# Kernel tuning notes

Measured on AMD Instinct MI355X. Metric: run time of the kernel, lower is better.

Reference implementation:

```python
import jax, jax.numpy as jnp
import numpy as np

T, B, S = 128, 128, 128
H, E, V, L = 1024, 512, 32000, 2


def setup_inputs() -> dict:
    key = jax.random.key(0)
    ks = jax.random.split(key, 16)
    s = 0.02
    inp = {
        "inputs": jax.random.randint(ks[0], (T, B), 0, V),
        "h0": jax.random.normal(ks[1], (L, B, H), jnp.float32) * 0.1,
        "c0": jax.random.normal(ks[2], (L, B, H), jnp.float32) * 0.1,
        "contexts": jax.random.normal(ks[3], (B, S, H), jnp.float32),
        "emb": jax.random.normal(ks[4], (V, E), jnp.float32) * s,
        "W_ih0": jax.random.normal(ks[5], (4 * H, E), jnp.float32) * s,
        "W_hh0": jax.random.normal(ks[6], (4 * H, H), jnp.float32) * s,
        "b_ih0": jnp.zeros((4 * H,), jnp.float32),
        "b_hh0": jnp.zeros((4 * H,), jnp.float32),
        "W_ih1": jax.random.normal(ks[7], (4 * H, H), jnp.float32) * s,
        "W_hh1": jax.random.normal(ks[8], (4 * H, H), jnp.float32) * s,
        "b_ih1": jnp.zeros((4 * H,), jnp.float32),
        "b_hh1": jnp.zeros((4 * H,), jnp.float32),
        "att_in_W": jax.random.normal(ks[9], (H, H), jnp.float32) * s,
        "att_in_b": jnp.zeros((H,), jnp.float32),
        "att_out_W": jax.random.normal(ks[10], (H, 2 * H), jnp.float32) * s,
        "att_out_b": jnp.zeros((H,), jnp.float32),
    }
    return inp


def _lstm_cell(x, h, c, Wih, Whh, bih, bhh):
    # torch.nn.LSTMCell: gates in (i, f, g, o) order
    gates = x @ Wih.T + bih + h @ Whh.T + bhh  # [B, 4H]
    i, f, g, o = jnp.split(gates, 4, axis=-1)
    c2 = jax.nn.sigmoid(f) * c + jax.nn.sigmoid(i) * jnp.tanh(g)
    h2 = jax.nn.sigmoid(o) * jnp.tanh(c2)
    return h2, c2


def reference(inputs, h0, c0, contexts, emb,
              W_ih0, W_hh0, b_ih0, b_hh0,
              W_ih1, W_hh1, b_ih1, b_hh1,
              att_in_W, att_in_b, att_out_W, att_out_b):
    layer_params = [(W_ih0, W_hh0, b_ih0, b_hh0), (W_ih1, W_hh1, b_ih1, b_hh1)]
    embs = emb[inputs]  # [T, B, E]

    def step(carry, x_t):
        h, c = carry  # each [L, B, H]
        x = x_t
        hs, cs = [], []
        for l, (Wih, Whh, bih, bhh) in enumerate(layer_params):
            h_l, c_l = _lstm_cell(x, h[l], c[l], Wih, Whh, bih, bhh)
            x = h_l  # dropout=0.0 / eval mode -> identity
            hs.append(h_l)
            cs.append(c_l)
        # global (Luong general) attention
        gamma = x @ att_in_W.T + att_in_b                     # [B, H]
        scores = jnp.einsum('bsh,bh->bs', contexts, gamma)    # [B, S]
        w = jax.nn.softmax(scores, axis=-1)
        c_t = jnp.einsum('bs,bsh->bh', w, contexts)           # [B, H]
        out = jnp.tanh(jnp.concatenate([c_t, x], axis=-1) @ att_out_W.T + att_out_b)
        return (jnp.stack(hs), jnp.stack(cs)), (out, w)

    (hT, cT), (outputs, attns) = jax.lax.scan(step, (h0, c0), embs)
    return outputs, hT, cT
```

## Files before the change

### kernel.cpp

```cpp
#include <hip/hip_runtime.h>

#define TT 128
#define BB 128
#define SS 128
#define HH 1024
#define EE 512
#define BH (BB*HH)

typedef unsigned short u16;
typedef unsigned long long u64;
typedef __attribute__((ext_vector_type(8))) short s8v;
typedef __attribute__((ext_vector_type(4))) float f32x4;

__device__ __forceinline__ float b2f(u16 u) {
    union { unsigned int i; float f; } v; v.i = ((unsigned int)u) << 16; return v.f;
}
__device__ __forceinline__ u16 f2b(float f) {
    union { float f; unsigned int i; } v; v.f = f;
    unsigned int x = v.i;
    x = x + 0x7fffu + ((x >> 16) & 1u);
    return (u16)(x >> 16);
}
__device__ __forceinline__ float sigm(float x) {
    float t = __expf(-fabsf(x));
    float p = 1.0f / (1.0f + t);
    return x >= 0.0f ? p : 1.0f - p;
}
__device__ __forceinline__ float tanh_(float x) {
    float t = __expf(-2.0f * fabsf(x));
    float r = (1.0f - t) / (1.0f + t);
    return x >= 0.0f ? r : -r;
}

#define MFMA(a, b, c) __builtin_amdgcn_mfma_f32_16x16x32_bf16((a), (b), (c), 0, 0, 0)

__global__ __launch_bounds__(256)
void cvt_k(const float* __restrict__ s, u16* __restrict__ d, int n)
{
    const int i = (blockIdx.x * 256 + threadIdx.x) * 4;
    if (i < n) {
        const float4 v = *(const float4*)(s + i);
        ushort4 o;
        o.x = f2b(v.x); o.y = f2b(v.y); o.z = f2b(v.z); o.w = f2b(v.w);
        *(ushort4*)(d + i) = o;
    }
}

__global__ __launch_bounds__(128)
void gather_k(const int* __restrict__ toks, const float* __restrict__ emb,
              u16* __restrict__ X)
{
    const int row = blockIdx.x;
    const int tok = toks[row];
    const int c = threadIdx.x * 4;
    const float4 v = *(const float4*)(emb + (size_t)tok * EE + c);
    ushort4 o;
    o.x = f2b(v.x); o.y = f2b(v.y); o.z = f2b(v.z); o.w = f2b(v.w);
    *(ushort4*)(X + (size_t)row * EE + c) = o;
}

__global__ __launch_bounds__(256)
void init_k(const float* __restrict__ h0in,
            u16* __restrict__ h0ring, u16* __restrict__ h1init,
            int* __restrict__ barcnt)
{
    const int i = blockIdx.x * 256 + threadIdx.x;
    const u16 hb = f2b(h0in[i]);
    if (i < BH) h0ring[i] = hb;
    else        h1init[i - BH] = hb;
    if (i < 256) barcnt[i] = 0;
}

__global__ __launch_bounds__(512, 1)
void scan_k(const float* __restrict__ Wih0, const float* __restrict__ Whh0,
            const float* __restrict__ Wih1, const float* __restrict__ Whh1,
            const float* __restrict__ bih0, const float* __restrict__ bhh0,
            const float* __restrict__ bih1, const float* __restrict__ bhh1,
            const float* __restrict__ c0in,
            const u16* __restrict__ Xb,
            u16* __restrict__ h0ring,
            const u16* __restrict__ h1init,
            u16* __restrict__ H1all,
            float* __restrict__ outT,
            int* __restrict__ barcnt)
{
    extern __shared__ u16 lds[];
    u16* W0x = lds;
    u16* W0h = W0x + 16*4*16*8;
    u16* W1x = W0h + 32*4*16*8;
    u16* W1h = W1x + 32*4*16*8;
    float* gst0 = (float*)(W1h + 32*4*16*8);
    float* gst1 = gst0 + 8*16*20;

    const int tid  = threadIdx.x;
    const int bk   = blockIdx.x;
    const int j0   = (((bk & 7) << 5) | (bk >> 3)) * 4;
    const int lane = tid & 63;
    const int w    = tid >> 6;
    const int l15  = lane & 15, quad = lane >> 4;

    auto loadW = [&](const float* src, int K, u16* dst) {
        const int ntup = (K / 32) * 4 * 16;
        for (int idx = tid; idx < ntup; idx += 512) {
            const int n = idx & 15, q = (idx >> 4) & 3, kc = idx >> 6;
            const int col = ((n >> 2) * HH) + j0 + (n & 3);
            const float* sp = src + (size_t)col * K + kc * 32 + q * 8;
            const float4 v0 = *(const float4*)(sp);
            const float4 v1 = *(const float4*)(sp + 4);
            u16* dp = dst + (size_t)idx * 8;
            dp[0] = f2b(v0.x); dp[1] = f2b(v0.y); dp[2] = f2b(v0.z); dp[3] = f2b(v0.w);
            dp[4] = f2b(v1.x); dp[5] = f2b(v1.y); dp[6] = f2b(v1.z); dp[7] = f2b(v1.w);
        }
    };
    loadW(Wih0, EE, W0x);
    loadW(Whh0, HH, W0h);
    loadW(Wih1, HH, W1x);
    loadW(Whh1, HH, W1h);

    const int pr = tid & 127;
    f32x4 cst = (f32x4)0.0f;
    f32x4 bs0 = (f32x4)0.0f, bs1 = (f32x4)0.0f, bs2 = (f32x4)0.0f, bs3 = (f32x4)0.0f;
    if (tid < 256) {
        const int layer = tid >> 7;
        const float* bi = layer ? bih1 : bih0;
        const float* bh = layer ? bhh1 : bhh0;
        cst = *(const f32x4*)(c0in + (size_t)layer * BH + (size_t)pr * HH + j0);
        bs0 = *(const f32x4*)(bi + 0 * HH + j0) + *(const f32x4*)(bh + 0 * HH + j0);
        bs1 = *(const f32x4*)(bi + 1 * HH + j0) + *(const f32x4*)(bh + 1 * HH + j0);
        bs2 = *(const f32x4*)(bi + 2 * HH + j0) + *(const f32x4*)(bh + 2 * HH + j0);
        bs3 = *(const f32x4*)(bi + 3 * HH + j0) + *(const f32x4*)(bh + 3 * HH + j0);
    }

    __syncthreads();

    const int arow = w * 16 + l15;

    #define BIDX(kc) (((size_t)((kc) * 4 + quad) * 16 + l15) * 8)

    auto pointwise = [&](const float* gbase, u16* dst, float* oH, float* oC,
                         bool doOut) {
        const float* gr = gbase + (pr >> 4) * 320 + (pr & 15) * 20;
        const f32x4 vi = *(const f32x4*)(gr + 0);
        const f32x4 vf = *(const f32x4*)(gr + 4);
        const f32x4 vg = *(const f32x4*)(gr + 8);
        const f32x4 vo = *(const f32x4*)(gr + 12);
        f32x4 hv;
        #pragma unroll
        for (int jj = 0; jj < 4; ++jj) {
            const float gi = vi[jj] + bs0[jj];
            const float gf = vf[jj] + bs1[jj];
            const float gg = vg[jj] + bs2[jj];
            const float go = vo[jj] + bs3[jj];
            const float c = sigm(gf) * cst[jj] + sigm(gi) * tanh_(gg);
            cst[jj] = c;
            hv[jj] = sigm(go) * tanh_(c);
        }
        const u64 pk = (u64)f2b(hv[0]) | ((u64)f2b(hv[1]) << 16)
                     | ((u64)f2b(hv[2]) << 32) | ((u64)f2b(hv[3]) << 48);
        __hip_atomic_store((u64*)(dst + (size_t)pr * HH + j0), pk,
                           __ATOMIC_RELAXED, __HIP_MEMORY_SCOPE_AGENT);
        if (doOut) {
            *(f32x4*)(oH + (size_t)pr * HH + j0) = hv;
            *(f32x4*)(oC + (size_t)pr * HH + j0) = cst;
        }
    };

    for (int p = 0; p <= TT; ++p) {
        f32x4 acc0 = (f32x4)0.0f, acc1 = (f32x4)0.0f;

        if (p < TT) {
            const u16* ap = Xb + ((size_t)p * BB + arow) * EE + quad * 8;
            #pragma unroll 8
            for (int kc = 0; kc < 16; ++kc) {
                s8v a = *(const s8v*)(ap + kc * 32);
                s8v b = *(const s8v*)(W0x + BIDX(kc));
                acc0 = MFMA(a, b, acc0);
            }
        }

        if (p > 0) {
            if (tid < 8) {
                const int target = 32 * p;
                while (__hip_atomic_load(barcnt + tid * 32, __ATOMIC_RELAXED,
                                         __HIP_MEMORY_SCOPE_AGENT) < target) {
                    __builtin_amdgcn_s_sleep(1);
                }
            }
            __syncthreads();
            asm volatile("" ::: "memory");
        }

        const u16* h0p = h0ring + (size_t)p * BH;
        const u16* a0p = h0p + (size_t)arow * HH + quad * 8;
        if (p == 0) {
            #pragma unroll 8
            for (int kc = 0; kc < 32; ++kc) {
                s8v a = *(const s8v*)(a0p + kc * 32);
                acc0 = MFMA(a, *(const s8v*)(W0h + BIDX(kc)), acc0);
            }
        } else {
            const u16* h1p = (p == 1) ? h1init : (H1all + (size_t)(p - 2) * BH);
            const u16* a1p = h1p + (size_t)arow * HH + quad * 8;
            if (p < TT) {
                #pragma unroll 8
                for (int kc = 0; kc < 32; ++kc) {
                    s8v a0 = *(const s8v*)(a0p + kc * 32);
                    s8v a1 = *(const s8v*)(a1p + kc * 32);
                    acc0 = MFMA(a0, *(const s8v*)(W0h + BIDX(kc)), acc0);
                    acc1 = MFMA(a0, *(const s8v*)(W1x + BIDX(kc)), acc1);
                    acc1 = MFMA(a1, *(const s8v*)(W1h + BIDX(kc)), acc1);
                }
            } else {
                #pragma unroll 8
                for (int kc = 0; kc < 32; ++kc) {
                    s8v a0 = *(const s8v*)(a0p + kc * 32);
                    s8v a1 = *(const s8v*)(a1p + kc * 32);
                    acc1 = MFMA(a0, *(const s8v*)(W1x + BIDX(kc)), acc1);
                    acc1 = MFMA(a1, *(const s8v*)(W1h + BIDX(kc)), acc1);
                }
            }
        }

        if (p < TT) {
            #pragma unroll
            for (int r = 0; r < 4; ++r)
                gst0[w * 320 + (quad * 4 + r) * 20 + l15] = acc0[r];
        }
        if (p > 0) {
            #pragma unroll
            for (int r = 0; r < 4; ++r)
                gst1[w * 320 + (quad * 4 + r) * 20 + l15] = acc1[r];
        }
        __syncthreads();
        if (p < TT && tid < 128)
            pointwise(gst0, h0ring + (size_t)(p + 1) * BH,
                      outT + (size_t)0 * BH, outT + (size_t)2 * BH, p == TT - 1);
        if (p > 0 && tid >= 128 && tid < 256)
            pointwise(gst1, H1all + (size_t)(p - 1) * BH,
                      outT + (size_t)1 * BH, outT + (size_t)3 * BH, p == TT);
        __syncthreads();

        if (p < TT && tid == 0) {
            __hip_atomic_fetch_add(barcnt + (bk & 7) * 32, 1, __ATOMIC_RELAXED,
                                   __HIP_MEMORY_SCOPE_AGENT);
        }
    }
    #undef BIDX
}

__global__ __launch_bounds__(256)
void gemm_bt_k(const u16* __restrict__ A1, int K1,
               const u16* __restrict__ A2, int K2,
               const u16* __restrict__ W, int ldw,
               const float* __restrict__ bias,
               u16* __restrict__ Cb, float* __restrict__ Cf,
               int N, int act)
{
    const int lane = threadIdx.x & 63;
    const int wave = threadIdx.x >> 6;
    const int l15 = lane & 15, quad = lane >> 4;
    const int n0 = blockIdx.x * 64;
    const int mrow = blockIdx.y * 64 + wave * 16;
    const int arow = mrow + l15;

    f32x4 acc[4];
    #pragma unroll
    for (int nt = 0; nt < 4; ++nt) acc[nt] = (f32x4)0.0f;

    const u16* wr0 = W + (size_t)(n0 + 0 * 16 + l15) * ldw + quad * 8;
    const u16* wr1 = W + (size_t)(n0 + 1 * 16 + l15) * ldw + quad * 8;
    const u16* wr2 = W + (size_t)(n0 + 2 * 16 + l15) * ldw + quad * 8;
    const u16* wr3 = W + (size_t)(n0 + 3 * 16 + l15) * ldw + quad * 8;

    {
        const u16* ap = A1 + (size_t)arow * K1 + quad * 8;
        #pragma unroll 4
        for (int kk = 0; kk < K1; kk += 32) {
            s8v a = *(const s8v*)(ap + kk);
            acc[0] = MFMA(a, *(const s8v*)(wr0 + kk), acc[0]);
            acc[1] = MFMA(a, *(const s8v*)(wr1 + kk), acc[1]);
            acc[2] = MFMA(a, *(const s8v*)(wr2 + kk), acc[2]);
            acc[3] = MFMA(a, *(const s8v*)(wr3 + kk), acc[3]);
        }
    }
    if (A2 != nullptr) {
        const u16* ap = A2 + (size_t)arow * K2 + quad * 8;
        #pragma unroll 4
        for (int kk = 0; kk < K2; kk += 32) {
            s8v a = *(const s8v*)(ap + kk);
            acc[0] = MFMA(a, *(const s8v*)(wr0 + K1 + kk), acc[0]);
            acc[1] = MFMA(a, *(const s8v*)(wr1 + K1 + kk), acc[1]);
            acc[2] = MFMA(a, *(const s8v*)(wr2 + K1 + kk), acc[2]);
            acc[3] = MFMA(a, *(const s8v*)(wr3 + K1 + kk), acc[3]);
        }
    }
    #pragma unroll
    for (int nt = 0; nt < 4; ++nt) {
        const int col = n0 + nt * 16 + l15;
        const float bv = bias[col];
        #pragma unroll
        for (int r = 0; r < 4; ++r) {
            const int row = mrow + quad * 4 + r;
            float v = acc[nt][r] + bv;
            if (act) v = tanh_(v);
            if (Cf) Cf[(size_t)row * N + col] = v;
            else    Cb[(size_t)row * N + col] = f2b(v);
        }
    }
}

__global__ __launch_bounds__(256)
void attn_k(const u16* __restrict__ gamma, const float* __restrict__ ctx,
            u16* __restrict__ ctall)
{
    const int b = blockIdx.x;
    const int t0 = blockIdx.y * 16;
    const int tid = threadIdx.x;
    const int lane = tid & 63, wave = tid >> 6;
    const int l15 = lane & 15, quad = lane >> 4;

    __shared__ float sw[16 * SS];

    {
        f32x4 acc0 = (f32x4)0.0f, acc1 = (f32x4)0.0f;
        const u16*   ap  = gamma + ((size_t)(t0 + l15) * BB + b) * HH + quad * 8;
        const float* bp0 = ctx + ((size_t)b * SS + (wave * 32 + l15)) * HH + quad * 8;
        const float* bp1 = ctx + ((size_t)b * SS + (wave * 32 + 16 + l15)) * HH + quad * 8;
        for (int kk = 0; kk < HH; kk += 32) {
            s8v a = *(const s8v*)(ap + kk);
            float4 u0 = *(const float4*)(bp0 + kk);
            float4 u1 = *(const float4*)(bp0 + kk + 4);
            s8v bv;
            bv[0] = (short)f2b(u0.x); bv[1] = (short)f2b(u0.y);
            bv[2] = (short)f2b(u0.z); bv[3] = (short)f2b(u0.w);
            bv[4] = (short)f2b(u1.x); bv[5] = (short)f2b(u1.y);
            bv[6] = (short)f2b(u1.z); bv[7] = (short)f2b(u1.w);
            acc0 = MFMA(a, bv, acc0);
            float4 w0 = *(const float4*)(bp1 + kk);
            float4 w1 = *(const float4*)(bp1 + kk + 4);
            s8v cv;
            cv[0] = (short)f2b(w0.x); cv[1] = (short)f2b(w0.y);
            cv[2] = (short)f2b(w0.z); cv[3] = (short)f2b(w0.w);
            cv[4] = (short)f2b(w1.x); cv[5] = (short)f2b(w1.y);
            cv[6] = (short)f2b(w1.z); cv[7] = (short)f2b(w1.w);
            acc1 = MFMA(a, cv, acc1);
        }
        #pragma unroll
        for (int r = 0; r < 4; ++r) {
            const int trow = quad * 4 + r;
            sw[trow * SS + wave * 32 + l15] = acc0[r];
            sw[trow * SS + wave * 32 + 16 + l15] = acc1[r];
        }
    }
    __syncthreads();

    {
        const int row = tid >> 4, c0 = tid & 15;
        float e[8];
        float m = -1e30f;
        #pragma unroll
        for (int k = 0; k < 8; ++k) { e[k] = sw[row * SS + c0 + k * 16]; m = fmaxf(m, e[k]); }
        #pragma unroll
        for (int off = 8; off >= 1; off >>= 1) m = fmaxf(m, __shfl_xor(m, off));
        float s = 0.0f;
        #pragma unroll
        for (int k = 0; k < 8; ++k) { e[k] = __expf(e[k] - m); s += e[k]; }
        #pragma unroll
        for (int off = 8; off >= 1; off >>= 1) s += __shfl_xor(s, off);
        const float inv = 1.0f / s;
        #pragma unroll
        for (int k = 0; k < 8; ++k) sw[row * SS + c0 + k * 16] = e[k] * inv;
    }
    __syncthreads();

    {
        const int h0 = tid * 4;
        float a[16][4];
        #pragma unroll
        for (int t = 0; t < 16; ++t)
            #pragma unroll
            for (int q = 0; q < 4; ++q) a[t][q] = 0.0f;

        const float* cp = ctx + (size_t)b * SS * HH + h0;
        for (int s = 0; s < SS; ++s) {
            const float4 cv = *(const float4*)(cp + (size_t)s * HH);
            #pragma unroll
            for (int t = 0; t < 16; ++t) {
                const float wgt = sw[t * SS + s];
                a[t][0] += wgt * cv.x;
                a[t][1] += wgt * cv.y;
                a[t][2] += wgt * cv.z;
                a[t][3] += wgt * cv.w;
            }
        }
        #pragma unroll
        for (int t = 0; t < 16; ++t) {
            u16* op = ctall + ((size_t)(t0 + t) * BB + b) * HH + h0;
            #pragma unroll
            for (int q = 0; q < 4; ++q) op[q] = f2b(a[t][q]);
        }
    }
}

extern "C" void kernel_launch(void* const* d_in, const int* in_sizes, int n_in,
                              void* d_out, int out_size, void* d_ws, size_t ws_size,
                              hipStream_t stream)
{
    const int*   toks = (const int*)d_in[0];
    const float* h0in = (const float*)d_in[1];
    const float* c0in = (const float*)d_in[2];
    const float* ctx  = (const float*)d_in[3];
    const float* emb  = (const float*)d_in[4];
    const float* Wih0 = (const float*)d_in[5];
    const float* Whh0 = (const float*)d_in[6];
    const float* bih0 = (const float*)d_in[7];
    const float* bhh0 = (const float*)d_in[8];
    const float* Wih1 = (const float*)d_in[9];
    const float* Whh1 = (const float*)d_in[10];
    const float* bih1 = (const float*)d_in[11];
    const float* bhh1 = (const float*)d_in[12];
    const float* attW = (const float*)d_in[13];
    const float* attb = (const float*)d_in[14];
    const float* outW = (const float*)d_in[15];
    const float* outb = (const float*)d_in[16];

    u16*   h0ring = (u16*)d_ws;
    u16*   h1init = h0ring + (size_t)(TT + 1) * BH;
    int*   barcnt = (int*)(h1init + BH);
    u16*   Xb     = (u16*)(barcnt + 256);
    u16*   H1all  = Xb + (size_t)TT * BB * EE;
    u16*   gammaA = H1all + (size_t)TT * BH;
    u16*   attWb  = gammaA + (size_t)TT * BH;
    u16*   outWb  = attWb + (size_t)HH * HH;
    u16*   ctall  = h0ring;

    cvt_k<<<dim3((HH * HH / 4 + 255) / 256), 256, 0, stream>>>(attW, attWb, HH * HH);
    cvt_k<<<dim3((2 * HH * HH / 4 + 255) / 256), 256, 0, stream>>>(outW, outWb, 2 * HH * HH);

    gather_k<<<dim3(TT * BB), 128, 0, stream>>>(toks, emb, Xb);
    init_k<<<dim3(2 * BH / 256), 256, 0, stream>>>(h0in, h0ring, h1init, barcnt);

    float* outp = (float*)d_out;
    const int ldsBytes = (16*4*16*8 + 3 * 32*4*16*8) * 2 + 2 * 8*16*20 * 4;
    hipFuncSetAttribute((const void*)scan_k,
                        hipFuncAttributeMaxDynamicSharedMemorySize, ldsBytes);
    scan_k<<<dim3(256), 512, ldsBytes, stream>>>(
        Wih0, Whh0, Wih1, Whh1, bih0, bhh0, bih1, bhh1, c0in,
        Xb, h0ring, h1init, H1all, outp + (size_t)TT * BH, barcnt);

    gemm_bt_k<<<dim3(HH / 64, (TT * BB) / 64), 256, 0, stream>>>(
        H1all, HH, nullptr, 0, attWb, HH, attb, gammaA, nullptr, HH, 0);

    attn_k<<<dim3(BB, TT / 16), 256, 0, stream>>>(gammaA, ctx, ctall);

    gemm_bt_k<<<dim3(HH / 64, (TT * BB) / 64), 256, 0, stream>>>(
        ctall, HH, H1all, HH, outWb, 2 * HH, outb, nullptr, outp, HH, 1);
}
```

Before: 3.706 ms.

## Split grid barrier into separate layer-0 and layer-1 barriers for earlier release

The single per-step grid barrier is replaced by two counters: one signals that the layer-0 hidden state is published, and the other that the layer-1 state is published. Each block now computes layer-0 gates, publishes h0 and signals barrier A before doing the layer-1 recurrent matmul, which waits only on barrier B from the previous step. Other blocks can therefore start the next layer-0 step while layer-1 work is still in flight, shortening the critical path. The cost is extra __syncthreads and spin-waits per step, a larger barrier-counter area, and more complex ordering of the cross-block dependencies.

```diff
diff --git a/kernel.cpp b/kernel.cpp
--- a/kernel.cpp
+++ b/kernel.cpp
@@ -68,7 +68,7 @@
     const u16 hb = f2b(h0in[i]);
     if (i < BH) h0ring[i] = hb;
     else        h1init[i - BH] = hb;
-    if (i < 256) barcnt[i] = 0;
+    if (i < 512) barcnt[i] = 0;
 }
 
 __global__ __launch_bounds__(512, 1)
@@ -99,6 +99,9 @@
     const int w    = tid >> 6;
     const int l15  = lane & 15, quad = lane >> 4;
 
+    int* barA = barcnt;
+    int* barB = barcnt + 256;
+
     auto loadW = [&](const float* src, int K, u16* dst) {
         const int ntup = (K / 32) * 4 * 16;
         for (int idx = tid; idx < ntup; idx += 512) {
@@ -173,15 +176,14 @@
             #pragma unroll 8
             for (int kc = 0; kc < 16; ++kc) {
                 s8v a = *(const s8v*)(ap + kc * 32);
-                s8v b = *(const s8v*)(W0x + BIDX(kc));
-                acc0 = MFMA(a, b, acc0);
+                acc0 = MFMA(a, *(const s8v*)(W0x + BIDX(kc)), acc0);
             }
         }
 
         if (p > 0) {
             if (tid < 8) {
                 const int target = 32 * p;
-                while (__hip_atomic_load(barcnt + tid * 32, __ATOMIC_RELAXED,
+                while (__hip_atomic_load(barA + tid * 32, __ATOMIC_RELAXED,
                                          __HIP_MEMORY_SCOPE_AGENT) < target) {
                     __builtin_amdgcn_s_sleep(1);
                 }
@@ -190,33 +192,20 @@
             asm volatile("" ::: "memory");
         }
 
-        const u16* h0p = h0ring + (size_t)p * BH;
-        const u16* a0p = h0p + (size_t)arow * HH + quad * 8;
-        if (p == 0) {
-            #pragma unroll 8
-            for (int kc = 0; kc < 32; ++kc) {
-                s8v a = *(const s8v*)(a0p + kc * 32);
-                acc0 = MFMA(a, *(const s8v*)(W0h + BIDX(kc)), acc0);
-            }
-        } else {
-            const u16* h1p = (p == 1) ? h1init : (H1all + (size_t)(p - 2) * BH);
-            const u16* a1p = h1p + (size_t)arow * HH + quad * 8;
+        {
+            const u16* a0p = h0ring + (size_t)p * BH + (size_t)arow * HH + quad * 8;
             if (p < TT) {
                 #pragma unroll 8
                 for (int kc = 0; kc < 32; ++kc) {
                     s8v a0 = *(const s8v*)(a0p + kc * 32);
-                    s8v a1 = *(const s8v*)(a1p + kc * 32);
                     acc0 = MFMA(a0, *(const s8v*)(W0h + BIDX(kc)), acc0);
                     acc1 = MFMA(a0, *(const s8v*)(W1x + BIDX(kc)), acc1);
-                    acc1 = MFMA(a1, *(const s8v*)(W1h + BIDX(kc)), acc1);
                 }
             } else {
                 #pragma unroll 8
                 for (int kc = 0; kc < 32; ++kc) {
                     s8v a0 = *(const s8v*)(a0p + kc * 32);
-                    s8v a1 = *(const s8v*)(a1p + kc * 32);
                     acc1 = MFMA(a0, *(const s8v*)(W1x + BIDX(kc)), acc1);
-                    acc1 = MFMA(a1, *(const s8v*)(W1h + BIDX(kc)), acc1);
                 }
             }
         }
@@ -226,24 +215,43 @@
             for (int r = 0; r < 4; ++r)
                 gst0[w * 320 + (quad * 4 + r) * 20 + l15] = acc0[r];
         }
-        if (p > 0) {
-            #pragma unroll
-            for (int r = 0; r < 4; ++r)
-                gst1[w * 320 + (quad * 4 + r) * 20 + l15] = acc1[r];
-        }
         __syncthreads();
         if (p < TT && tid < 128)
             pointwise(gst0, h0ring + (size_t)(p + 1) * BH,
                       outT + (size_t)0 * BH, outT + (size_t)2 * BH, p == TT - 1);
+        if (p >= 2 && tid >= 256 && tid < 264) {
+            const int target = 32 * (p - 1);
+            while (__hip_atomic_load(barB + (tid - 256) * 32, __ATOMIC_RELAXED,
+                                     __HIP_MEMORY_SCOPE_AGENT) < target) {
+                __builtin_amdgcn_s_sleep(1);
+            }
+        }
+        __syncthreads();
+        asm volatile("" ::: "memory");
+        if (p < TT && tid == 0)
+            __hip_atomic_fetch_add(barA + (bk & 7) * 32, 1, __ATOMIC_RELAXED,
+                                   __HIP_MEMORY_SCOPE_AGENT);
+
+        if (p > 0) {
+            const u16* h1p = (p == 1) ? h1init : (H1all + (size_t)(p - 2) * BH);
+            const u16* a1p = h1p + (size_t)arow * HH + quad * 8;
+            #pragma unroll 8
+            for (int kc = 0; kc < 32; ++kc) {
+                s8v a1 = *(const s8v*)(a1p + kc * 32);
+                acc1 = MFMA(a1, *(const s8v*)(W1h + BIDX(kc)), acc1);
+            }
+            #pragma unroll
+            for (int r = 0; r < 4; ++r)
+                gst1[w * 320 + (quad * 4 + r) * 20 + l15] = acc1[r];
+        }
+        __syncthreads();
         if (p > 0 && tid >= 128 && tid < 256)
             pointwise(gst1, H1all + (size_t)(p - 1) * BH,
                       outT + (size_t)1 * BH, outT + (size_t)3 * BH, p == TT);
         __syncthreads();
-
-        if (p < TT && tid == 0) {
-            __hip_atomic_fetch_add(barcnt + (bk & 7) * 32, 1, __ATOMIC_RELAXED,
+        if (p > 0 && tid == 0)
+            __hip_atomic_fetch_add(barB + (bk & 7) * 32, 1, __ATOMIC_RELAXED,
                                    __HIP_MEMORY_SCOPE_AGENT);
-        }
     }
     #undef BIDX
 }
@@ -427,7 +435,7 @@
     u16*   h0ring = (u16*)d_ws;
     u16*   h1init = h0ring + (size_t)(TT + 1) * BH;
     int*   barcnt = (int*)(h1init + BH);
-    u16*   Xb     = (u16*)(barcnt + 256);
+    u16*   Xb     = (u16*)(barcnt + 512);
     u16*   H1all  = Xb + (size_t)TT * BB * EE;
     u16*   gammaA = H1all + (size_t)TT * BH;
     u16*   attWb  = gammaA + (size_t)TT * BH;
```

Measured after the change: 3.841 ms. 1.04x slower.
